# Kernel optimization log

Measured on AMD Instinct MI355X. Metric: run time of the kernel, lower is better.

The kernel has to match this reference:

```python
import jax, jax.numpy as jnp
import numpy as np

B, L, D, H, DFF = 8, 1024, 256, 8, 2048
DH = D // H


def setup_inputs() -> dict:
    key = jax.random.key(0)
    ks = jax.random.split(key, 12)

    def w(k, shape):
        return jax.random.normal(k, shape, dtype=jnp.float32) * 0.02

    # continuous padding: first `length` tokens valid, rest padded (mask True = pad)
    lengths = jax.random.randint(ks[0], (B,), L // 4, L + 1)
    mask = jnp.arange(L)[None, :] >= lengths[:, None]

    return {
        "src": jax.random.normal(ks[1], (B, L, D), dtype=jnp.float32),
        "src_key_padding_mask": mask,
        "in_proj_w": w(ks[2], (3 * D, D)),
        "in_proj_b": w(ks[3], (3 * D,)),
        "out_w": w(ks[4], (D, D)),
        "out_b": w(ks[5], (D,)),
        "proj_w": w(ks[6], (D, D)),
        "proj_b": w(ks[7], (D,)),
        "ff1_w": w(ks[8], (DFF, D)),
        "ff1_b": w(ks[9], (DFF,)),
        "ff2_w": w(ks[10], (D, DFF)),
        "ff2_b": w(ks[11], (D,)),
    }


def reference(src, src_key_padding_mask, in_proj_w, in_proj_b, out_w, out_b,
              proj_w, proj_b, ff1_w, ff1_b, ff2_w, ff2_b):
    mask = src_key_padding_mask  # [B, L], True = padding
    neg_inf = jnp.float32(-jnp.inf)

    # --- make_attn_mask (vectorized, continuous padding) ---
    s = (~mask).sum(axis=1).astype(jnp.float32)              # [B] valid lengths
    idx = jnp.arange(L, dtype=jnp.float32)
    dist = jnp.abs(idx[:, None] - idx[None, :])              # [L, L]
    valid_tok = idx[None, :] < s[:, None]                    # [B, L]
    pair_ok = valid_tok[:, :, None] & valid_tok[:, None, :]  # [B, L, L]
    bias = jnp.where(pair_ok, (s[:, None, None] - dist[None]) / s[:, None, None], neg_inf)
    # rows that are entirely -inf (padded query rows) are zeroed, like masked_fill
    row_pad = ~valid_tok                                     # [B, L]
    bias = jnp.where(row_pad[:, :, None], 0.0, bias)
    # key_padding_mask is merged additively (as in nn.MultiheadAttention)
    add_mask = bias + jnp.where(mask[:, None, :], neg_inf, 0.0)  # [B, L, L]

    # --- multi-head self-attention ---
    qkv = src @ in_proj_w.T + in_proj_b                      # [B, L, 3D]
    q, k, v = jnp.split(qkv, 3, axis=-1)

    def heads(t):
        return t.reshape(B, L, H, DH).transpose(0, 2, 1, 3)  # [B, H, L, DH]

    q, k, v = heads(q), heads(k), heads(v)
    scale = 1.0 / jnp.sqrt(jnp.float32(DH))
    scores = jnp.einsum('bhqd,bhkd->bhqk', q, k) * scale + add_mask[:, None]
    attn = jax.nn.softmax(scores, axis=-1)
    ctx = jnp.einsum('bhqk,bhkd->bhqd', attn, v)
    ctx = ctx.transpose(0, 2, 1, 3).reshape(B, L, D)
    h_attn = ctx @ out_w.T + out_b

    # --- residual proj + FFN (no layernorm, no dropout) ---
    h = src + (h_attn @ proj_w.T + proj_b)
    ff = jax.nn.gelu(h @ ff1_w.T + ff1_b, approximate=False) @ ff2_w.T + ff2_b
    h = h + ff

    # zero out padded rows (masked_fill with all_neg_inf)
    h = jnp.where(row_pad[:, :, None], 0.0, h)
    return h
```

## Files before the change

### kernel.cpp

```cpp
#include <hip/hip_runtime.h>
#include <hip/hip_bf16.h>


#define BB   8
#define LL   1024
#define DD   256
#define HHN  8
#define DHH  32
#define DFFN 2048

typedef __attribute__((ext_vector_type(8))) __bf16 bf16x8;
typedef __attribute__((ext_vector_type(4))) float f32x4;

__device__ inline void gload16(const void* g, void* l) {
  __builtin_amdgcn_global_load_lds(
      (const __attribute__((address_space(1))) void*)g,
      (__attribute__((address_space(3))) void*)l, 16, 0, 0);
}

__device__ inline bf16x8 cvt8(const float4 a, const float4 b) {
  bf16x8 o;
  o[0] = (__bf16)a.x; o[1] = (__bf16)a.y; o[2] = (__bf16)a.z; o[3] = (__bf16)a.w;
  o[4] = (__bf16)b.x; o[5] = (__bf16)b.y; o[6] = (__bf16)b.z; o[7] = (__bf16)b.w;
  return o;
}

__device__ inline void cvt_block(const float* __restrict__ s,
                                 __hip_bfloat16* __restrict__ d, int i0) {
  const int i = i0 + threadIdx.x * 8;
  const float4 a = *(const float4*)(s + i);
  const float4 b = *(const float4*)(s + i + 4);
  *(bf16x8*)(d + i) = cvt8(a, b);
}

#define NB_WC   128
#define NB_QKV  768
#define BID_QKV  NB_WC
#define BID_LENS (NB_WC + NB_QKV)
#define NB_K1    (BID_LENS + 1)

__global__ __launch_bounds__(256) void fused_pre_qkv(
    const float* __restrict__ src, const unsigned char* __restrict__ mb,
    const float* __restrict__ in_proj_w, const float* __restrict__ in_proj_b,
    const float* __restrict__ proj_w, const float* __restrict__ out_w,
    const float* __restrict__ proj_b, const float* __restrict__ out_b,
    __hip_bfloat16* __restrict__ qkv_bf, __hip_bfloat16* __restrict__ wc_bf,
    float* __restrict__ bc, int* __restrict__ lens) {
  __shared__ __bf16 As[2][64][32];
  __shared__ __bf16 Bs[2][128][32];
  __shared__ float red[256];
  __shared__ float pw[2][256];
  __shared__ int cnt8[BB];
  __shared__ int flag3f, flagNA;

  const int bid = blockIdx.x;
  const int tid = threadIdx.x;

  if (bid < NB_WC) {
    const int i0 = bid << 1;
    const int k = tid;
    pw[0][k] = proj_w[(size_t)i0 * DD + k];
    pw[1][k] = proj_w[(size_t)(i0 + 1) * DD + k];
    __syncthreads();
    float a0 = 0.f, a1 = 0.f;
#pragma unroll 8
    for (int n = 0; n < DD; ++n) {
      const float won = out_w[n * DD + k];
      a0 = fmaf(pw[0][n], won, a0);
      a1 = fmaf(pw[1][n], won, a1);
    }
    wc_bf[(size_t)i0 * DD + k] = (__hip_bfloat16)a0;
    wc_bf[(size_t)(i0 + 1) * DD + k] = (__hip_bfloat16)a1;
#pragma unroll
    for (int j = 0; j < 2; ++j) {
      red[k] = pw[j][k] * out_b[k];
      __syncthreads();
      for (int sft = 128; sft > 0; sft >>= 1) {
        if (k < sft) red[k] += red[k + sft];
        __syncthreads();
      }
      if (k == 0) bc[i0 + j] = proj_b[i0 + j] + red[0];
      __syncthreads();
    }
  } else if (bid < BID_LENS) {
    const int qb = bid - BID_QKV;
    const int x = qb % 6;
    const int y = qb / 6;
    const int c0 = x << 7;
    const int r0 = y << 6;
    const int w = tid >> 6;
    const int lane = tid & 63;
    const int c = lane & 15;
    const int hq = lane >> 4;
    const int h8 = hq << 3;
    const int wr = w >> 1, wc2 = w & 1;
    const int srow = tid >> 2;
    const int scol = (tid & 3) << 3;

    float4 ra[2], rb[2][2];
    auto LOADR = [&](int kt) {
      const int k0 = kt << 5;
      const float* ap = src + (size_t)(r0 + srow) * DD + k0 + scol;
      ra[0] = *(const float4*)ap;
      ra[1] = *(const float4*)(ap + 4);
#pragma unroll
      for (int ch = 0; ch < 2; ++ch) {
        const float* wp =
            in_proj_w + (size_t)(c0 + (ch << 6) + srow) * DD + k0 + scol;
        rb[ch][0] = *(const float4*)wp;
        rb[ch][1] = *(const float4*)(wp + 4);
      }
    };
    auto WRITEL = [&](int buf) {
      *(bf16x8*)&As[buf][srow][scol] = cvt8(ra[0], ra[1]);
#pragma unroll
      for (int ch = 0; ch < 2; ++ch)
        *(bf16x8*)&Bs[buf][(ch << 6) + srow][scol] = cvt8(rb[ch][0], rb[ch][1]);
    };

    f32x4 acc[2][4];
#pragma unroll
    for (int m = 0; m < 2; ++m)
#pragma unroll
      for (int n = 0; n < 4; ++n) acc[m][n] = (f32x4){0.f, 0.f, 0.f, 0.f};

    int buf = 0;
    LOADR(0);
    WRITEL(0);
    __syncthreads();
    for (int kt = 0; kt < 8; ++kt) {
      if (kt + 1 < 8) LOADR(kt + 1);
      bf16x8 af[2], bfr[4];
#pragma unroll
      for (int m = 0; m < 2; ++m)
        af[m] = *(const bf16x8*)&As[buf][wr * 32 + (m << 4) + c][h8];
#pragma unroll
      for (int n = 0; n < 4; ++n)
        bfr[n] = *(const bf16x8*)&Bs[buf][(wc2 << 6) + (n << 4) + c][h8];
#pragma unroll
      for (int m = 0; m < 2; ++m)
#pragma unroll
        for (int n = 0; n < 4; ++n)
          acc[m][n] = __builtin_amdgcn_mfma_f32_16x16x32_bf16(af[m], bfr[n],
                                                              acc[m][n], 0, 0, 0);
      if (kt + 1 < 8) WRITEL(buf ^ 1);
      __syncthreads();
      buf ^= 1;
    }

    float bv[4];
#pragma unroll
    for (int n = 0; n < 4; ++n)
      bv[n] = in_proj_b[c0 + (wc2 << 6) + (n << 4) + c];
#pragma unroll
    for (int m = 0; m < 2; ++m)
#pragma unroll
      for (int i = 0; i < 4; ++i) {
        const int gr = r0 + wr * 32 + (m << 4) + (hq << 2) + i;
#pragma unroll
        for (int n = 0; n < 4; ++n)
          qkv_bf[(size_t)gr * 768 + c0 + (wc2 << 6) + (n << 4) + c] =
              (__hip_bfloat16)(acc[m][n][i] + bv[n]);
      }
  } else {
    if (tid == 0) { flag3f = 0; flagNA = 0; }
    if (tid < BB) cnt8[tid] = 0;
    __syncthreads();
    for (int i = tid; i < BB * LL; i += 256) {
      unsigned char v = mb[i];
      if (v) {
        if ((i & 3) == 3 && v == 0x3F) flag3f = 1;
        else if (i & 3) flagNA = 1;
      }
    }
    __syncthreads();
    const bool isfloat = (flag3f != 0);
    const bool isbool = (!isfloat) && (flagNA != 0);
    if (isbool) {
      for (int i = tid; i < BB * LL; i += 256)
        if (mb[i] == 0) atomicAdd(&cnt8[i >> 10], 1);
    } else {
      const int* mi = (const int*)mb;
      for (int i = tid; i < BB * LL; i += 256)
        if (mi[i] == 0) atomicAdd(&cnt8[i >> 10], 1);
    }
    __syncthreads();
    if (tid < BB) lens[tid] = cnt8[tid];
  }
}

template <int EPI, int BM, int BN>
__device__ __forceinline__ void gemm_body(
    const __hip_bfloat16* __restrict__ A, const __hip_bfloat16* __restrict__ W,
    const float* __restrict__ bias, const float* __restrict__ resid,
    float* __restrict__ Cf, __hip_bfloat16* __restrict__ Cb, const int N,
    const int K, const int* __restrict__ lens, const int bx, const int by) {
  constexpr int MF = BM / 32;
  constexpr int NF = BN / 32;
  constexpr int CHA = BM / 64;
  constexpr int CHB = BN / 64;
  __shared__ __bf16 As[2][BM][32];
  __shared__ __bf16 Bs[2][BN][32];

  const int tid = threadIdx.x;
  const int w = tid >> 6;
  const int lane = tid & 63;
  const int c = lane & 15;
  const int hq = lane >> 4;
  const int h8 = hq << 3;
  const int wr = w >> 1, wc = w & 1;
  const int c0 = bx * BN;
  const int r0 = by * BM;
  if ((r0 & (LL - 1)) >= lens[r0 >> 10]) return;

  const int srow = tid >> 2;
  const int scol = (tid & 3) << 3;

  auto STAGE = [&](int buf, int kt) {
    const int k0 = kt << 5;
#pragma unroll
    for (int ch = 0; ch < CHA; ++ch)
      gload16(A + (size_t)(r0 + (ch << 6) + srow) * K + k0 + scol,
              &As[buf][(ch << 6) + (w << 4)][0]);
#pragma unroll
    for (int ch = 0; ch < CHB; ++ch)
      gload16(W + (size_t)(c0 + (ch << 6) + srow) * K + k0 + scol,
              &Bs[buf][(ch << 6) + (w << 4)][0]);
  };

  f32x4 acc[MF][NF];
#pragma unroll
  for (int m = 0; m < MF; ++m)
#pragma unroll
    for (int n = 0; n < NF; ++n) acc[m][n] = (f32x4){0.f, 0.f, 0.f, 0.f};

  const int nkt = K >> 5;
  int buf = 0;
  STAGE(0, 0);
  __syncthreads();
  for (int kt = 0; kt < nkt; ++kt) {
    if (kt + 1 < nkt) STAGE(buf ^ 1, kt + 1);
    bf16x8 af[MF], bfr[NF];
#pragma unroll
    for (int m = 0; m < MF; ++m)
      af[m] = *(const bf16x8*)&As[buf][wr * (MF * 16) + (m << 4) + c][h8];
#pragma unroll
    for (int n = 0; n < NF; ++n)
      bfr[n] = *(const bf16x8*)&Bs[buf][wc * (NF * 16) + (n << 4) + c][h8];
#pragma unroll
    for (int m = 0; m < MF; ++m)
#pragma unroll
      for (int n = 0; n < NF; ++n)
        acc[m][n] =
            __builtin_amdgcn_mfma_f32_16x16x32_bf16(af[m], bfr[n], acc[m][n], 0, 0, 0);
    __syncthreads();
    buf ^= 1;
  }

  float bv[NF];
#pragma unroll
  for (int n = 0; n < NF; ++n) bv[n] = bias[c0 + wc * (NF * 16) + (n << 4) + c];

#pragma unroll
  for (int m = 0; m < MF; ++m) {
#pragma unroll
    for (int i = 0; i < 4; ++i) {
      const int gr = r0 + wr * (MF * 16) + (m << 4) + (hq << 2) + i;
#pragma unroll
      for (int n = 0; n < NF; ++n) {
        const int gc = c0 + wc * (NF * 16) + (n << 4) + c;
        float v = acc[m][n][i] + bv[n];
        if (EPI == 1) v = 0.5f * v * (1.0f + erff(v * 0.70710678118654752f));
        if (EPI == 2) {
          v += resid[(size_t)gr * N + gc];
          Cf[(size_t)gr * N + gc] = v;
        }
        Cb[(size_t)gr * N + gc] = (__hip_bfloat16)v;
      }
    }
  }
}

__global__ __launch_bounds__(256) void proj_cvt(
    const __hip_bfloat16* __restrict__ ctx, const __hip_bfloat16* __restrict__ wc,
    const float* __restrict__ bc, const float* __restrict__ src,
    float* __restrict__ hbuf_f, __hip_bfloat16* __restrict__ hbuf_bf,
    const int* __restrict__ lens, const float* __restrict__ ff1_w,
    __hip_bfloat16* __restrict__ wff1_bf) {
  const int bid = blockIdx.x;
  if (bid < 512) {
    gemm_body<2, 64, 64>(ctx, wc, bc, src, hbuf_f, hbuf_bf, DD, DD, lens,
                         bid & 3, bid >> 2);
  } else {
    cvt_block(ff1_w, wff1_bf, (bid - 512) * 2048);
  }
}

__global__ __launch_bounds__(256) void ff1_cvt(
    const __hip_bfloat16* __restrict__ hbuf_bf,
    const __hip_bfloat16* __restrict__ wff1_bf, const float* __restrict__ ff1_b,
    __hip_bfloat16* __restrict__ ff1o_bf, const int* __restrict__ lens,
    const float* __restrict__ ff2_w, __hip_bfloat16* __restrict__ wff2_bf) {
  const int bid = blockIdx.x;
  if (bid < 1024) {
    gemm_body<1, 128, 128>(hbuf_bf, wff1_bf, ff1_b, nullptr, nullptr, ff1o_bf,
                           DFFN, DD, lens, bid & 15, bid >> 4);
  } else {
    cvt_block(ff2_w, wff2_bf, (bid - 1024) * 2048);
  }
}

__global__ __launch_bounds__(256) void gemm_ff2_part(
    const __hip_bfloat16* __restrict__ A, const __hip_bfloat16* __restrict__ W,
    __hip_bfloat16* __restrict__ P, const int* __restrict__ lens) {
  __shared__ __bf16 As[2][64][32];
  __shared__ __bf16 Bs[2][128][32];

  const int tid = threadIdx.x;
  const int w = tid >> 6;
  const int lane = tid & 63;
  const int c = lane & 15;
  const int hq = lane >> 4;
  const int h8 = hq << 3;
  const int wr = w >> 1, wc = w & 1;
  const int c0 = blockIdx.x << 7;
  const int r0 = blockIdx.y << 6;
  if ((r0 & (LL - 1)) >= lens[r0 >> 10]) return;

  const int kz = blockIdx.z;
  const int kbase = kz << 9;
  const int srow = tid >> 2;
  const int scol = (tid & 3) << 3;

  auto STAGE = [&](int buf, int kt) {
    const int k0 = kbase + (kt << 5);
    gload16(A + (size_t)(r0 + srow) * DFFN + k0 + scol, &As[buf][w << 4][0]);
#pragma unroll
    for (int ch = 0; ch < 2; ++ch)
      gload16(W + (size_t)(c0 + (ch << 6) + srow) * DFFN + k0 + scol,
              &Bs[buf][(ch << 6) + (w << 4)][0]);
  };

  f32x4 acc[2][4];
#pragma unroll
  for (int m = 0; m < 2; ++m)
#pragma unroll
    for (int n = 0; n < 4; ++n) acc[m][n] = (f32x4){0.f, 0.f, 0.f, 0.f};

  int buf = 0;
  STAGE(0, 0);
  __syncthreads();
  for (int kt = 0; kt < 16; ++kt) {
    if (kt + 1 < 16) STAGE(buf ^ 1, kt + 1);
    bf16x8 af[2], bfr[4];
#pragma unroll
    for (int m = 0; m < 2; ++m)
      af[m] = *(const bf16x8*)&As[buf][wr * 32 + (m << 4) + c][h8];
#pragma unroll
    for (int n = 0; n < 4; ++n)
      bfr[n] = *(const bf16x8*)&Bs[buf][(wc << 6) + (n << 4) + c][h8];
#pragma unroll
    for (int m = 0; m < 2; ++m)
#pragma unroll
      for (int n = 0; n < 4; ++n)
        acc[m][n] =
            __builtin_amdgcn_mfma_f32_16x16x32_bf16(af[m], bfr[n], acc[m][n], 0, 0, 0);
    __syncthreads();
    buf ^= 1;
  }

  __hip_bfloat16* Pz = P + (size_t)kz * (BB * LL) * DD;
#pragma unroll
  for (int m = 0; m < 2; ++m)
#pragma unroll
    for (int i = 0; i < 4; ++i) {
      const int gr = r0 + wr * 32 + (m << 4) + (hq << 2) + i;
#pragma unroll
      for (int n = 0; n < 4; ++n)
        Pz[(size_t)gr * DD + c0 + (wc << 6) + (n << 4) + c] =
            (__hip_bfloat16)acc[m][n][i];
    }
}

__global__ __launch_bounds__(256) void ff2_reduce(
    const __hip_bfloat16* __restrict__ P, const float* __restrict__ resid,
    const float* __restrict__ bias, float* __restrict__ out,
    const int* __restrict__ lens) {
  const int idx = blockIdx.x * 256 + threadIdx.x;
  const int r = idx >> 6;
  const int c4 = (idx & 63) << 2;
  float4 o;
  if ((r & (LL - 1)) >= lens[r >> 10]) {
    o.x = o.y = o.z = o.w = 0.f;
  } else {
    const size_t base = (size_t)r * DD + c4;
    o = *(const float4*)&resid[base];
    const float4 bv = *(const float4*)&bias[c4];
    o.x += bv.x; o.y += bv.y; o.z += bv.z; o.w += bv.w;
#pragma unroll
    for (int z = 0; z < 4; ++z) {
      const ushort4 pu = *(const ushort4*)(P + (size_t)z * (BB * LL) * DD + base);
      o.x += __bfloat162float(*(const __hip_bfloat16*)&pu.x);
      o.y += __bfloat162float(*(const __hip_bfloat16*)&pu.y);
      o.z += __bfloat162float(*(const __hip_bfloat16*)&pu.z);
      o.w += __bfloat162float(*(const __hip_bfloat16*)&pu.w);
    }
  }
  *(float4*)&out[(size_t)r * DD + c4] = o;
}

__global__ __launch_bounds__(256) void attn_fwd_mfma(
    const __hip_bfloat16* __restrict__ qkv, __hip_bfloat16* __restrict__ ctx,
    const int* __restrict__ lens) {
  __shared__ __bf16 Ks[2][64][56];
  __shared__ __bf16 Vt[2][32][66];
  __shared__ __bf16 Pl[4][16][72];

  const int tid = threadIdx.x;
  const int q0 = blockIdx.x << 6;
  const int hh = blockIdx.y;
  const int b = blockIdx.z;
  const int slen = lens[b];
  if (q0 >= slen) return;

  const int w = tid >> 6;
  const int lane = tid & 63;
  const int c = lane & 15;
  const int h = lane >> 4;
  const int h8 = h << 3;

  const float L2E = 1.44269504f;
  const float sf = (float)slen;
  const float cb = -7.0f * L2E;
  const float cd = (1.0f / sf) * L2E;
  const float qscale = 0.17677669529663689f * L2E;

  bf16x8 qf;
  {
    const int qrow = q0 + (w << 4) + c;
    const bf16x8 qraw =
        *(const bf16x8*)(qkv + (size_t)(b * LL + qrow) * 768 + hh * DHH + h8);
#pragma unroll
    for (int j = 0; j < 8; ++j) qf[j] = (__bf16)((float)qraw[j] * qscale);
  }

  f32x4 acc0 = {0.f, 0.f, 0.f, 0.f};
  f32x4 acc1 = {0.f, 0.f, 0.f, 0.f};
  float lsum[4] = {0.f, 0.f, 0.f, 0.f};

  const int skey = tid >> 2;
  const int sdg = (tid & 3) << 3;
  const int ntk = (slen + 63) >> 6;
  const int qg = q0 + (w << 4) + (h << 2);

  const __hip_bfloat16* kvbase = qkv + (size_t)b * LL * 768 + 256 + hh * DHH + sdg;

  bf16x8 kreg, vreg;
  {
    const __hip_bfloat16* kb = kvbase + (size_t)skey * 768;
    kreg = *(const bf16x8*)kb;
    vreg = *(const bf16x8*)(kb + 256);
    *(bf16x8*)&Ks[0][skey][sdg] = kreg;
#pragma unroll
    for (int j = 0; j < 8; ++j) Vt[0][sdg + j][skey] = vreg[j];
  }
  if (ntk > 1) {
    const __hip_bfloat16* kb = kvbase + (size_t)(64 + skey) * 768;
    kreg = *(const bf16x8*)kb;
    vreg = *(const bf16x8*)(kb + 256);
  }
  __syncthreads();

  for (int kt = 0; kt < ntk; ++kt) {
    const int p = kt & 1;
    const int kbase = kt << 6;

    f32x4 st[4];
    __builtin_amdgcn_s_setprio(1);
#pragma unroll
    for (int t = 0; t < 4; ++t) {
      const bf16x8 kf = *(const bf16x8*)&Ks[p][(t << 4) + c][h8];
      st[t] = __builtin_amdgcn_mfma_f32_16x16x32_bf16(
          qf, kf, (f32x4){0.f, 0.f, 0.f, 0.f}, 0, 0, 0);
    }
    __builtin_amdgcn_s_setprio(0);

    if (kbase + 64 <= slen) {
#pragma unroll
      for (int t = 0; t < 4; ++t) {
        const float kjf = (float)(kbase + (t << 4) + c);
#pragma unroll
        for (int i = 0; i < 4; ++i) {
          const float dist = fabsf((float)(qg + i) - kjf);
          const float pv = __builtin_amdgcn_exp2f(st[t][i] + cb - dist * cd);
          lsum[i] += pv;
          Pl[w][(h << 2) + i][c + (t << 4)] = (__bf16)pv;
        }
      }
    } else {
#pragma unroll
      for (int t = 0; t < 4; ++t) {
        const int kj = kbase + (t << 4) + c;
        const bool kvalid = kj < slen;
        const float kjf = (float)kj;
#pragma unroll
        for (int i = 0; i < 4; ++i) {
          const float dist = fabsf((float)(qg + i) - kjf);
          const float arg = kvalid ? (st[t][i] + cb - dist * cd) : -1e30f;
          const float pv = __builtin_amdgcn_exp2f(arg);
          lsum[i] += pv;
          Pl[w][(h << 2) + i][c + (t << 4)] = (__bf16)pv;
        }
      }
    }

    asm volatile("s_waitcnt lgkmcnt(0)" ::: "memory");

    __builtin_amdgcn_s_setprio(1);
#pragma unroll
    for (int n = 0; n < 2; ++n) {
      const bf16x8 pf = *(const bf16x8*)&Pl[w][c][h8 + (n << 5)];
      const uint32_t* v0p = (const uint32_t*)&Vt[p][c][h8 + (n << 5)];
      const uint32_t* v1p = (const uint32_t*)&Vt[p][16 + c][h8 + (n << 5)];
      union { uint32_t u[4]; bf16x8 v; } t0, t1;
#pragma unroll
      for (int j = 0; j < 4; ++j) { t0.u[j] = v0p[j]; t1.u[j] = v1p[j]; }
      acc0 = __builtin_amdgcn_mfma_f32_16x16x32_bf16(pf, t0.v, acc0, 0, 0, 0);
      acc1 = __builtin_amdgcn_mfma_f32_16x16x32_bf16(pf, t1.v, acc1, 0, 0, 0);
    }
    __builtin_amdgcn_s_setprio(0);

    if (kt + 1 < ntk) {
      *(bf16x8*)&Ks[p ^ 1][skey][sdg] = kreg;
#pragma unroll
      for (int j = 0; j < 8; ++j) Vt[p ^ 1][sdg + j][skey] = vreg[j];
      if (kt + 2 < ntk) {
        const __hip_bfloat16* kb = kvbase + (size_t)(((kt + 2) << 6) + skey) * 768;
        kreg = *(const bf16x8*)kb;
        vreg = *(const bf16x8*)(kb + 256);
      }
    }
    __syncthreads();
  }

#pragma unroll
  for (int i = 0; i < 4; ++i) {
    float l = lsum[i];
    l += __shfl_xor(l, 1);
    l += __shfl_xor(l, 2);
    l += __shfl_xor(l, 4);
    l += __shfl_xor(l, 8);
    const float il = 1.0f / l;
    __hip_bfloat16* op =
        ctx + (size_t)(b * LL + q0 + (w << 4) + (h << 2) + i) * 256 + hh * DHH;
    op[c] = (__hip_bfloat16)(acc0[i] * il);
    op[c + 16] = (__hip_bfloat16)(acc1[i] * il);
  }
}

extern "C" void kernel_launch(void* const* d_in, const int* in_sizes, int n_in,
                              void* d_out, int out_size, void* d_ws,
                              size_t ws_size, hipStream_t stream) {
  (void)in_sizes; (void)n_in; (void)out_size; (void)ws_size;
  const float* src = (const float*)d_in[0];
  const unsigned char* mask = (const unsigned char*)d_in[1];
  const float* in_proj_w = (const float*)d_in[2];
  const float* in_proj_b = (const float*)d_in[3];
  const float* out_w = (const float*)d_in[4];
  const float* out_b = (const float*)d_in[5];
  const float* proj_w = (const float*)d_in[6];
  const float* proj_b = (const float*)d_in[7];
  const float* ff1_w = (const float*)d_in[8];
  const float* ff1_b = (const float*)d_in[9];
  const float* ff2_w = (const float*)d_in[10];
  const float* ff2_b = (const float*)d_in[11];
  float* out = (float*)d_out;

  const int M = BB * LL;
  char* p = (char*)d_ws;
  __hip_bfloat16* qkv_bf = (__hip_bfloat16*)p; p += (size_t)M * 768 * 2;
  __hip_bfloat16* ctx_bf = (__hip_bfloat16*)p; p += (size_t)M * 256 * 2;
  float* hbuf_f = (float*)p;                    p += (size_t)M * 256 * 4;
  __hip_bfloat16* hbuf_bf = (__hip_bfloat16*)p; p += (size_t)M * 256 * 2;
  __hip_bfloat16* ff1o_bf = (__hip_bfloat16*)p; p += (size_t)M * 2048 * 2;
  __hip_bfloat16* wff1_bf = (__hip_bfloat16*)p; p += (size_t)2048 * 256 * 2;
  __hip_bfloat16* wff2_bf = (__hip_bfloat16*)p; p += (size_t)256 * 2048 * 2;
  __hip_bfloat16* wc_bf = (__hip_bfloat16*)p;   p += (size_t)256 * 256 * 2;
  float* bc = (float*)p;                        p += 256 * 4;
  int* lens = (int*)p;                          p += 256;
  __hip_bfloat16* pbuf = (__hip_bfloat16*)p;    p += (size_t)4 * M * 256 * 2;

  fused_pre_qkv<<<NB_K1, 256, 0, stream>>>(src, mask, in_proj_w, in_proj_b,
                                           proj_w, out_w, proj_b, out_b,
                                           qkv_bf, wc_bf, bc, lens);

  attn_fwd_mfma<<<dim3(LL / 64, HHN, BB), 256, 0, stream>>>(qkv_bf, ctx_bf, lens);

  proj_cvt<<<768, 256, 0, stream>>>(ctx_bf, wc_bf, bc, src, hbuf_f, hbuf_bf,
                                    lens, ff1_w, wff1_bf);

  ff1_cvt<<<1280, 256, 0, stream>>>(hbuf_bf, wff1_bf, ff1_b, ff1o_bf, lens,
                                    ff2_w, wff2_bf);

  gemm_ff2_part<<<dim3(2, 128, 4), 256, 0, stream>>>(ff1o_bf, wff2_bf, pbuf, lens);

  ff2_reduce<<<M * 256 / 4 / 256, 256, 0, stream>>>(pbuf, hbuf_f, ff2_b, out, lens);
}
```

Baseline: 115.6 us.

## Swizzle GEMM block ids across XCDs and drop fp32 residual buffer

Adds an XCD-aware block-index swizzle to the QKV, proj, FF1 and FF2 GEMM grids so that neighbouring tiles land on the same chiplet and share its L2. The FF2 grid is flattened to 1D so the swizzle can apply there too. It also removes the fp32 copy of the post-attention hidden state and has the final reduce read the bf16 copy as the residual, which cuts one fp32 write and read of M×256. The trade-off is that the residual now carries bf16 rounding, which lowers output accuracy.

```diff
diff --git a/kernel.cpp b/kernel.cpp
--- a/kernel.cpp
+++ b/kernel.cpp
@@ -31,6 +31,10 @@
   const float4 a = *(const float4*)(s + i);
   const float4 b = *(const float4*)(s + i + 4);
   *(bf16x8*)(d + i) = cvt8(a, b);
+}
+
+__device__ inline int xcd_swz(int bid, int nwg) {
+  return (bid & 7) * (nwg >> 3) + (bid >> 3);
 }
 
 #define NB_WC   128
@@ -83,7 +87,7 @@
       __syncthreads();
     }
   } else if (bid < BID_LENS) {
-    const int qb = bid - BID_QKV;
+    const int qb = xcd_swz(bid - BID_QKV, NB_QKV);
     const int x = qb % 6;
     const int y = qb / 6;
     const int c0 = x << 7;
@@ -193,8 +197,8 @@
 __device__ __forceinline__ void gemm_body(
     const __hip_bfloat16* __restrict__ A, const __hip_bfloat16* __restrict__ W,
     const float* __restrict__ bias, const float* __restrict__ resid,
-    float* __restrict__ Cf, __hip_bfloat16* __restrict__ Cb, const int N,
-    const int K, const int* __restrict__ lens, const int bx, const int by) {
+    __hip_bfloat16* __restrict__ Cb, const int N, const int K,
+    const int* __restrict__ lens, const int bx, const int by) {
   constexpr int MF = BM / 32;
   constexpr int NF = BN / 32;
   constexpr int CHA = BM / 64;
@@ -271,10 +275,7 @@
         const int gc = c0 + wc * (NF * 16) + (n << 4) + c;
         float v = acc[m][n][i] + bv[n];
         if (EPI == 1) v = 0.5f * v * (1.0f + erff(v * 0.70710678118654752f));
-        if (EPI == 2) {
-          v += resid[(size_t)gr * N + gc];
-          Cf[(size_t)gr * N + gc] = v;
-        }
+        if (EPI == 2) v += resid[(size_t)gr * N + gc];
         Cb[(size_t)gr * N + gc] = (__hip_bfloat16)v;
       }
     }
@@ -284,13 +285,12 @@
 __global__ __launch_bounds__(256) void proj_cvt(
     const __hip_bfloat16* __restrict__ ctx, const __hip_bfloat16* __restrict__ wc,
     const float* __restrict__ bc, const float* __restrict__ src,
-    float* __restrict__ hbuf_f, __hip_bfloat16* __restrict__ hbuf_bf,
-    const int* __restrict__ lens, const float* __restrict__ ff1_w,
-    __hip_bfloat16* __restrict__ wff1_bf) {
+    __hip_bfloat16* __restrict__ hbuf_bf, const int* __restrict__ lens,
+    const float* __restrict__ ff1_w, __hip_bfloat16* __restrict__ wff1_bf) {
   const int bid = blockIdx.x;
   if (bid < 512) {
-    gemm_body<2, 64, 64>(ctx, wc, bc, src, hbuf_f, hbuf_bf, DD, DD, lens,
-                         bid & 3, bid >> 2);
+    const int t = xcd_swz(bid, 512);
+    gemm_body<2, 64, 64>(ctx, wc, bc, src, hbuf_bf, DD, DD, lens, t & 3, t >> 2);
   } else {
     cvt_block(ff1_w, wff1_bf, (bid - 512) * 2048);
   }
@@ -303,8 +303,9 @@
     const float* __restrict__ ff2_w, __hip_bfloat16* __restrict__ wff2_bf) {
   const int bid = blockIdx.x;
   if (bid < 1024) {
-    gemm_body<1, 128, 128>(hbuf_bf, wff1_bf, ff1_b, nullptr, nullptr, ff1o_bf,
-                           DFFN, DD, lens, bid & 15, bid >> 4);
+    const int t = xcd_swz(bid, 1024);
+    gemm_body<1, 128, 128>(hbuf_bf, wff1_bf, ff1_b, nullptr, ff1o_bf, DFFN, DD,
+                           lens, t & 15, t >> 4);
   } else {
     cvt_block(ff2_w, wff2_bf, (bid - 1024) * 2048);
   }
@@ -315,6 +316,11 @@
     __hip_bfloat16* __restrict__ P, const int* __restrict__ lens) {
   __shared__ __bf16 As[2][64][32];
   __shared__ __bf16 Bs[2][128][32];
+
+  const int t = xcd_swz(blockIdx.x, 1024);
+  const int kz = t >> 8;
+  const int y = (t & 255) >> 1;
+  const int x = t & 1;
 
   const int tid = threadIdx.x;
   const int w = tid >> 6;
@@ -323,11 +329,10 @@
   const int hq = lane >> 4;
   const int h8 = hq << 3;
   const int wr = w >> 1, wc = w & 1;
-  const int c0 = blockIdx.x << 7;
-  const int r0 = blockIdx.y << 6;
+  const int c0 = x << 7;
+  const int r0 = y << 6;
   if ((r0 & (LL - 1)) >= lens[r0 >> 10]) return;
 
-  const int kz = blockIdx.z;
   const int kbase = kz << 9;
   const int srow = tid >> 2;
   const int scol = (tid & 3) << 3;
@@ -383,7 +388,7 @@
 }
 
 __global__ __launch_bounds__(256) void ff2_reduce(
-    const __hip_bfloat16* __restrict__ P, const float* __restrict__ resid,
+    const __hip_bfloat16* __restrict__ P, const __hip_bfloat16* __restrict__ resid,
     const float* __restrict__ bias, float* __restrict__ out,
     const int* __restrict__ lens) {
   const int idx = blockIdx.x * 256 + threadIdx.x;
@@ -394,9 +399,12 @@
     o.x = o.y = o.z = o.w = 0.f;
   } else {
     const size_t base = (size_t)r * DD + c4;
-    o = *(const float4*)&resid[base];
+    const ushort4 rv = *(const ushort4*)(resid + base);
     const float4 bv = *(const float4*)&bias[c4];
-    o.x += bv.x; o.y += bv.y; o.z += bv.z; o.w += bv.w;
+    o.x = __bfloat162float(*(const __hip_bfloat16*)&rv.x) + bv.x;
+    o.y = __bfloat162float(*(const __hip_bfloat16*)&rv.y) + bv.y;
+    o.z = __bfloat162float(*(const __hip_bfloat16*)&rv.z) + bv.z;
+    o.w = __bfloat162float(*(const __hip_bfloat16*)&rv.w) + bv.w;
 #pragma unroll
     for (int z = 0; z < 4; ++z) {
       const ushort4 pu = *(const ushort4*)(P + (size_t)z * (BB * LL) * DD + base);
@@ -580,7 +588,6 @@
   char* p = (char*)d_ws;
   __hip_bfloat16* qkv_bf = (__hip_bfloat16*)p; p += (size_t)M * 768 * 2;
   __hip_bfloat16* ctx_bf = (__hip_bfloat16*)p; p += (size_t)M * 256 * 2;
-  float* hbuf_f = (float*)p;                    p += (size_t)M * 256 * 4;
   __hip_bfloat16* hbuf_bf = (__hip_bfloat16*)p; p += (size_t)M * 256 * 2;
   __hip_bfloat16* ff1o_bf = (__hip_bfloat16*)p; p += (size_t)M * 2048 * 2;
   __hip_bfloat16* wff1_bf = (__hip_bfloat16*)p; p += (size_t)2048 * 256 * 2;
@@ -596,13 +603,14 @@
 
   attn_fwd_mfma<<<dim3(LL / 64, HHN, BB), 256, 0, stream>>>(qkv_bf, ctx_bf, lens);
 
-  proj_cvt<<<768, 256, 0, stream>>>(ctx_bf, wc_bf, bc, src, hbuf_f, hbuf_bf,
-                                    lens, ff1_w, wff1_bf);
+  proj_cvt<<<768, 256, 0, stream>>>(ctx_bf, wc_bf, bc, src, hbuf_bf, lens,
+                                    ff1_w, wff1_bf);
 
   ff1_cvt<<<1280, 256, 0, stream>>>(hbuf_bf, wff1_bf, ff1_b, ff1o_bf, lens,
                                     ff2_w, wff2_bf);
 
-  gemm_ff2_part<<<dim3(2, 128, 4), 256, 0, stream>>>(ff1o_bf, wff2_bf, pbuf, lens);
-
-  ff2_reduce<<<M * 256 / 4 / 256, 256, 0, stream>>>(pbuf, hbuf_f, ff2_b, out, lens);
-}
+  gemm_ff2_part<<<1024, 256, 0, stream>>>(ff1o_bf, wff2_bf, pbuf, lens);
+
+  ff2_reduce<<<M * 256 / 4 / 256, 256, 0, stream>>>(pbuf, hbuf_bf, ff2_b, out,
+                                                    lens);
+}
```

Result: faster. 107.5 us (-7.1%).
